# Performance work log

Measured on AMD Instinct MI355X. Metric: run time of the kernel, lower is better.

The kernel has to match this reference:

```python
import jax, jax.numpy as jnp
import numpy as np

B, N, L = 4, 64, 64
D_MODEL = 128
D_INNER = 256   # expand=2
D_STATE = 16
D_CONV = 4
DT_RANK = 8     # ceil(D_MODEL/16)
N_LAYERS = 4
EPS = 1e-5


def setup_inputs() -> dict:
    key = jax.random.key(0)
    ks = jax.random.split(key, 16)
    f = jnp.float32
    s = 0.05
    return {
        'mha_in': jax.random.normal(ks[0], (B, N, L, D_MODEL), f),
        'mamba_mask': jax.random.bernoulli(ks[1], 0.9, (B, N, L)),
        'mlp_w1': jax.random.normal(ks[2], (D_MODEL, D_MODEL), f) * s,
        'mlp_b1': jnp.zeros((D_MODEL,), f),
        'mlp_w2': jax.random.normal(ks[3], (D_MODEL, D_MODEL), f) * s,
        'mlp_b2': jnp.zeros((D_MODEL,), f),
        'in_proj_w': jax.random.normal(ks[4], (N_LAYERS, 2 * D_INNER, D_MODEL), f) * s,
        'conv_w': jax.random.normal(ks[5], (N_LAYERS, D_INNER, D_CONV), f) * s,
        'conv_b': jnp.zeros((N_LAYERS, D_INNER), f),
        'x_proj_w': jax.random.normal(ks[6], (N_LAYERS, DT_RANK + 2 * D_STATE, D_INNER), f) * s,
        'dt_proj_w': jax.random.normal(ks[7], (N_LAYERS, D_INNER, DT_RANK), f) * s,
        'dt_proj_b': jax.random.uniform(ks[8], (N_LAYERS, D_INNER), f, -4.0, -2.0),
        'A_log': jnp.log(jnp.broadcast_to(jnp.arange(1, D_STATE + 1, dtype=f), (N_LAYERS, D_INNER, D_STATE))),
        'D_skip': jnp.ones((N_LAYERS, D_INNER), f),
        'out_proj_w': jax.random.normal(ks[9], (N_LAYERS, D_MODEL, D_INNER), f) * s,
        'blk_norm_w': jnp.ones((N_LAYERS, D_MODEL), f),
        'norm_f_w': jnp.ones((D_MODEL,), f),
    }


def rmsnorm(x, w):
    # fused add-RMSNorm keeps residual in fp32; weight multiply after normalize
    x32 = x.astype(jnp.float32)
    return (x32 * jax.lax.rsqrt(jnp.mean(x32 * x32, -1, keepdims=True) + EPS)) * w


def causal_conv1d(x, w, b):
    # x: [R, L, d_inner]; depthwise causal conv (torch conv1d, padding=D_CONV-1, truncated to L)
    xp = jnp.pad(x, ((0, 0), (D_CONV - 1, 0), (0, 0)))
    y = jnp.zeros_like(x) + b
    for k in range(D_CONV):
        y = y + w[:, k] * xp[:, k:k + L, :]
    return y


def selective_scan(u, dt, A, Bm, Cm, D_sk):
    # u, dt: [R, L, d_inner]; A: [d_inner, n]; Bm, Cm: [R, L, n]
    def step(h, inputs):
        dt_t, B_t, C_t, u_t = inputs  # [R,di], [R,n], [R,n], [R,di]
        dA = jnp.exp(dt_t[..., None] * A)                       # [R,di,n]
        h = dA * h + (dt_t * u_t)[..., None] * B_t[:, None, :]  # [R,di,n]
        y = jnp.einsum('rdn,rn->rd', h, C_t)
        return h, y
    h0 = jnp.zeros((u.shape[0], A.shape[0], A.shape[1]), u.dtype)
    xs = (dt.swapaxes(0, 1), Bm.swapaxes(0, 1), Cm.swapaxes(0, 1), u.swapaxes(0, 1))
    _, ys = jax.lax.scan(step, h0, xs)
    return ys.swapaxes(0, 1) + u * D_sk


def mamba_mixer(x, in_w, conv_w, conv_b, xproj_w, dt_w, dt_b, A_log, D_sk, out_w):
    xz = x @ in_w.T                             # [R,L,2*d_inner]
    xc, z = jnp.split(xz, 2, axis=-1)
    xc = jax.nn.silu(causal_conv1d(xc, conv_w, conv_b))
    x_dbl = xc @ xproj_w.T                      # [R,L,dt_rank+2n]
    dt = jax.nn.softplus(x_dbl[..., :DT_RANK] @ dt_w.T + dt_b)
    Bm = x_dbl[..., DT_RANK:DT_RANK + D_STATE]
    Cm = x_dbl[..., DT_RANK + D_STATE:]
    A = -jnp.exp(A_log)
    y = selective_scan(xc, dt, A, Bm, Cm, D_sk)
    return (y * jax.nn.silu(z)) @ out_w.T


def _forward(mha_in, mamba_mask, mlp_w1, mlp_b1, mlp_w2, mlp_b2, in_proj_w, conv_w,
             conv_b, x_proj_w, dt_proj_w, dt_proj_b, A_log, D_skip, out_proj_w,
             blk_norm_w, norm_f_w):
    R = B * N
    x = mha_in.reshape(R, L, D_MODEL)
    key_valid = jnp.any(mamba_mask.reshape(R, L), axis=-1)
    # hist_embed_mlp: Linear -> GELU(exact) -> Linear
    h = jax.nn.gelu(x @ mlp_w1.T + mlp_b1, approximate=False) @ mlp_w2.T + mlp_b2
    residual = None
    for i in range(N_LAYERS):
        residual = h if residual is None else h + residual  # fused add (fp32 residual)
        hn = rmsnorm(residual, blk_norm_w[i])
        h = mamba_mixer(hn, in_proj_w[i], conv_w[i], conv_b[i], x_proj_w[i],
                        dt_proj_w[i], dt_proj_b[i], A_log[i], D_skip[i], out_proj_w[i])
    residual = h + residual
    out = rmsnorm(residual, norm_f_w)            # prenorm=False final fused add-norm
    # scatter into zeros over valid rows == mask-multiply (rows independent)
    out = out * key_valid[:, None, None].astype(out.dtype)
    out = out.reshape(B, N, L, D_MODEL)
    return out[:, 0, -1, :]                      # ag_feat[:, -1, :]


def reference(mha_in, mamba_mask, mlp_w1, mlp_b1, mlp_w2, mlp_b2, in_proj_w, conv_w,
              conv_b, x_proj_w, dt_proj_w, dt_proj_b, A_log, D_skip, out_proj_w,
              blk_norm_w, norm_f_w):
    return _forward(mha_in, mamba_mask, mlp_w1, mlp_b1, mlp_w2, mlp_b2, in_proj_w,
                    conv_w, conv_b, x_proj_w, dt_proj_w, dt_proj_b, A_log, D_skip,
                    out_proj_w, blk_norm_w, norm_f_w)
```

## Files before the change

### kernel.cpp

```cpp
#include <hip/hip_runtime.h>
#include <math.h>

#define NWG  64
#define NTHR 512

#define WS_XG 512
#define WS_DT (WS_XG + 65536)
#define WS_DU (WS_DT + 65536)
#define WS_BC (WS_DU + 65536)
#define WS_Y  (WS_BC + 8192)

__device__ __forceinline__ float silu_f(float v) { return v / (1.0f + __expf(-v)); }
__device__ __forceinline__ float dot4(float4 a, float4 b) {
    return a.x*b.x + a.y*b.y + a.z*b.z + a.w*b.w;
}
__device__ __forceinline__ float wave_red_sum(float v) {
    v += __shfl_xor(v, 1);  v += __shfl_xor(v, 2);  v += __shfl_xor(v, 4);
    v += __shfl_xor(v, 8);  v += __shfl_xor(v, 16); v += __shfl_xor(v, 32);
    return v;
}
__device__ __forceinline__ float aload(const float* p) {
    return __hip_atomic_load(p, __ATOMIC_RELAXED, __HIP_MEMORY_SCOPE_AGENT);
}
__device__ __forceinline__ void astore(float* p, float v) {
    __hip_atomic_store(p, v, __ATOMIC_RELAXED, __HIP_MEMORY_SCOPE_AGENT);
}

__device__ __forceinline__ void seq_barrier(unsigned* slot) {
    __syncthreads();
    if (threadIdx.x == 0) {
        asm volatile("s_waitcnt vmcnt(0)" ::: "memory");
        __hip_atomic_fetch_add(slot, 1u, __ATOMIC_RELAXED, __HIP_MEMORY_SCOPE_AGENT);
        while (__hip_atomic_load(slot, __ATOMIC_RELAXED, __HIP_MEMORY_SCOPE_AGENT) < 16u)
            __builtin_amdgcn_s_sleep(1);
    }
    __syncthreads();
}

__global__ __launch_bounds__(NTHR, 1) void fused_kernel(
    const float* __restrict__ mha_in, const int* __restrict__ mask,
    const float* __restrict__ mlp_w1, const float* __restrict__ mlp_b1,
    const float* __restrict__ mlp_w2, const float* __restrict__ mlp_b2,
    const float* __restrict__ in_proj_w, const float* __restrict__ conv_w,
    const float* __restrict__ conv_b, const float* __restrict__ x_proj_w,
    const float* __restrict__ dt_proj_w, const float* __restrict__ dt_proj_b,
    const float* __restrict__ A_log, const float* __restrict__ D_skip,
    const float* __restrict__ out_proj_w, const float* __restrict__ blk_norm_w,
    const float* __restrict__ norm_f_w,
    float* __restrict__ ws, float* __restrict__ out)
{
    const int wg = blockIdx.x;
    const int t  = threadIdx.x;
    const int s  = wg & 3;
    const int rb = wg >> 2;
    const int l0 = rb * 4;
    const int r0 = s*64 + l0;
    const int d0 = rb * 16;
    const int h  = t >> 7;
    const int c  = t & 127;
    const int wave = t >> 6;

    unsigned* bar = (unsigned*)ws;
    float* xg  = ws + WS_XG;
    float* dtg = ws + WS_DT;
    float* dug = ws + WS_DU;
    float* bcg = ws + WS_BC;
    float* yg  = ws + WS_Y;

    __shared__ float bufX[4][256];
    __shared__ float bufZ[4][256];
    __shared__ float bufA[4][256];
    __shared__ float bufG[4][256];
    __shared__ float bufB[4][128];
    __shared__ float xdS[4][40];
    __shared__ float sdt[64][17];
    __shared__ float sdu[64][17];
    __shared__ float sbc[64][33];
    __shared__ float pOut[4][4][128];
    __shared__ float part[8];
    __shared__ int   anyv;

    float resid;

    bufB[h][c] = mha_in[(size_t)s*524288 + (size_t)(l0 + h)*128 + c];
    __syncthreads();
    {
        const float* w = mlp_w1 + (size_t)c * 128;
        float acc = 0.f;
        #pragma unroll 16
        for (int k4 = 0; k4 < 32; ++k4)
            acc += dot4(*(const float4*)&bufB[h][k4*4], *(const float4*)&w[k4*4]);
        float v = acc + mlp_b1[c];
        v = 0.5f*v*(1.0f + erff(v*0.70710678118f));
        bufA[h][c] = v;
    }
    __syncthreads();
    {
        const float* w = mlp_w2 + (size_t)c * 128;
        float acc = 0.f;
        #pragma unroll 16
        for (int k4 = 0; k4 < 32; ++k4)
            acc += dot4(*(const float4*)&bufA[h][k4*4], *(const float4*)&w[k4*4]);
        resid = acc + mlp_b2[c];
    }
    __syncthreads();

    for (int layer = 0; layer < 4; ++layer) {
        unsigned* s1slot = bar + (layer*4 + s)*16;
        unsigned* s2slot = bar + 256 + layer*4 + s;
        unsigned* s3slot = bar + 272 + layer*4 + s;

        {
            float sq = wave_red_sum(resid*resid);
            if ((t & 63) == 0) part[wave] = sq;
        }
        __syncthreads();
        {
            float sr = part[h*2] + part[h*2 + 1];
            float sc = rsqrtf(sr*(1.0f/128.0f) + 1e-5f);
            bufB[h][c] = resid * sc * blk_norm_w[layer*128 + c];
        }
        __syncthreads();

        {
            const int d = t & 255, hp = t >> 8;
            const float* w = in_proj_w + ((size_t)layer*512 + d)*128;
            float a0 = 0.f, a1 = 0.f;
            #pragma unroll 16
            for (int k4 = 0; k4 < 32; ++k4) {
                float4 wv = *(const float4*)&w[k4*4];
                a0 += dot4(*(const float4*)&bufB[hp*2  ][k4*4], wv);
                a1 += dot4(*(const float4*)&bufB[hp*2+1][k4*4], wv);
            }
            bufX[hp*2  ][d] = a0;
            bufX[hp*2+1][d] = a1;
            astore(&xg[(size_t)(r0 + hp*2    )*256 + d], a0);
            astore(&xg[(size_t)(r0 + hp*2 + 1)*256 + d], a1);
        }
        __syncthreads();
        if (t == 0) {
            asm volatile("s_waitcnt vmcnt(0)" ::: "memory");
            __hip_atomic_fetch_add(s1slot + rb, 1u, __ATOMIC_RELAXED, __HIP_MEMORY_SCOPE_AGENT);
            if (rb > 0) {
                while (__hip_atomic_load(s1slot + rb - 1, __ATOMIC_RELAXED, __HIP_MEMORY_SCOPE_AGENT) == 0u)
                    __builtin_amdgcn_s_sleep(1);
            }
        }
        __syncthreads();

        {
            int d = t & 255, half = t >> 8;
            int rbase = s*64;
            float4 cw = *(const float4*)&conv_w[((size_t)layer*256 + d)*4];
            float cb = conv_b[layer*256 + d];
            if (half == 0) {
                float x0 = (l0-3 >= 0) ? aload(&xg[(size_t)(rbase+l0-3)*256 + d]) : 0.f;
                float x1 = (l0-2 >= 0) ? aload(&xg[(size_t)(rbase+l0-2)*256 + d]) : 0.f;
                float x2 = (l0-1 >= 0) ? aload(&xg[(size_t)(rbase+l0-1)*256 + d]) : 0.f;
                float x3 = bufX[0][d];
                float x4 = bufX[1][d];
                bufA[0][d] = silu_f(cb + cw.x*x0 + cw.y*x1 + cw.z*x2 + cw.w*x3);
                bufA[1][d] = silu_f(cb + cw.x*x1 + cw.y*x2 + cw.z*x3 + cw.w*x4);
            } else {
                float x0 = (l0-1 >= 0) ? aload(&xg[(size_t)(rbase+l0-1)*256 + d]) : 0.f;
                float x1 = bufX[0][d];
                float x2 = bufX[1][d];
                float x3 = bufX[2][d];
                float x4 = bufX[3][d];
                bufA[2][d] = silu_f(cb + cw.x*x0 + cw.y*x1 + cw.z*x2 + cw.w*x3);
                bufA[3][d] = silu_f(cb + cw.x*x1 + cw.y*x2 + cw.z*x3 + cw.w*x4);
            }
        }
        __syncthreads();

        if (t < 160) {
            int rq = t & 3, jx = t >> 2;
            const float* xw = x_proj_w + ((size_t)layer*40 + jx)*256;
            float acc = 0.f;
            #pragma unroll 16
            for (int k4 = 0; k4 < 64; ++k4)
                acc += dot4(*(const float4*)&bufA[rq][k4*4], *(const float4*)&xw[k4*4]);
            xdS[rq][jx] = acc;
            if (jx >= 8)
                astore(&bcg[(size_t)(r0+rq)*32 + (jx-8)], acc);
        }
        __syncthreads();

        {
            int d = t & 255, half = t >> 8;
            const float* dw = dt_proj_w + ((size_t)layer*256 + d)*8;
            float4 wa = *(const float4*)&dw[0];
            float4 wb = *(const float4*)&dw[4];
            float b = dt_proj_b[layer*256 + d];
            #pragma unroll
            for (int q = 0; q < 2; ++q) {
                int rloc = half*2 + q;
                float4 xa = *(const float4*)&xdS[rloc][0];
                float4 xb = *(const float4*)&xdS[rloc][4];
                float pre = b + dot4(xa, wa) + dot4(xb, wb);
                float sp = (pre > 20.f) ? pre : log1pf(__expf(pre));
                astore(&dtg[(size_t)(r0+rloc)*256 + d], sp);
                astore(&dug[(size_t)(r0+rloc)*256 + d], sp * bufA[rloc][d]);
            }
        }
        seq_barrier(s2slot);

        if (t < 256) {
            int l = t >> 2, q = t & 3;
            const float* p = &dtg[(size_t)(s*64+l)*256 + d0 + q*4];
            sdt[l][q*4]   = aload(p);     sdt[l][q*4+1] = aload(p+1);
            sdt[l][q*4+2] = aload(p+2);   sdt[l][q*4+3] = aload(p+3);
        } else {
            int tt = t - 256; int l = tt >> 2, q = tt & 3;
            const float* p = &dug[(size_t)(s*64+l)*256 + d0 + q*4];
            sdu[l][q*4]   = aload(p);     sdu[l][q*4+1] = aload(p+1);
            sdu[l][q*4+2] = aload(p+2);   sdu[l][q*4+3] = aload(p+3);
        }
        {
            int l = t >> 3, q = t & 7;
            const float* p = &bcg[(size_t)(s*64+l)*32 + q*4];
            sbc[l][q*4]   = aload(p);     sbc[l][q*4+1] = aload(p+1);
            sbc[l][q*4+2] = aload(p+2);   sbc[l][q*4+3] = aload(p+3);
        }
        __syncthreads();

        if (t < 64) {
            const int dloc = t >> 2, sub = t & 3, d = d0 + dloc;
            const float* Ab = A_log + ((size_t)layer*256 + d)*16 + sub*4;
            float A0 = -__expf(Ab[0]), A1 = -__expf(Ab[1]);
            float A2 = -__expf(Ab[2]), A3 = -__expf(Ab[3]);
            float h0 = 0.f, h1v = 0.f, h2v = 0.f, h3v = 0.f;
            #pragma unroll 4
            for (int l = 0; l < 64; ++l) {
                float dtv = sdt[l][dloc];
                float duv = sdu[l][dloc];
                float4 B4, C4;
                B4.x = sbc[l][sub*4];      B4.y = sbc[l][sub*4+1];
                B4.z = sbc[l][sub*4+2];    B4.w = sbc[l][sub*4+3];
                C4.x = sbc[l][16+sub*4];   C4.y = sbc[l][16+sub*4+1];
                C4.z = sbc[l][16+sub*4+2]; C4.w = sbc[l][16+sub*4+3];
                float dA, yp;
                dA = __expf(dtv*A0); h0  = dA*h0  + duv*B4.x; yp  = h0 *C4.x;
                dA = __expf(dtv*A1); h1v = dA*h1v + duv*B4.y; yp += h1v*C4.y;
                dA = __expf(dtv*A2); h2v = dA*h2v + duv*B4.z; yp += h2v*C4.z;
                dA = __expf(dtv*A3); h3v = dA*h3v + duv*B4.w; yp += h3v*C4.w;
                yp += __shfl_xor(yp, 1);
                yp += __shfl_xor(yp, 2);
                if (sub == 0) astore(&yg[(size_t)(s*64+l)*256 + d], yp);
            }
        } else if (t >= 256) {
            const int dz = t - 256;
            const float* w = in_proj_w + ((size_t)layer*512 + 256 + dz)*128;
            float a0=0.f, a1=0.f, a2=0.f, a3=0.f;
            #pragma unroll 16
            for (int k4 = 0; k4 < 32; ++k4) {
                float4 wv = *(const float4*)&w[k4*4];
                a0 += dot4(*(const float4*)&bufB[0][k4*4], wv);
                a1 += dot4(*(const float4*)&bufB[1][k4*4], wv);
                a2 += dot4(*(const float4*)&bufB[2][k4*4], wv);
                a3 += dot4(*(const float4*)&bufB[3][k4*4], wv);
            }
            bufZ[0][dz] = a0;  bufZ[1][dz] = a1;
            bufZ[2][dz] = a2;  bufZ[3][dz] = a3;
        }
        seq_barrier(s3slot);

        {
            int d = t & 255, half = t >> 8;
            float Dsk = D_skip[layer*256 + d];
            #pragma unroll
            for (int q = 0; q < 2; ++q) {
                int rloc = half*2 + q; int r = r0 + rloc;
                float z = bufZ[rloc][d];
                float yv = aload(&yg[(size_t)r*256 + d]) + bufA[rloc][d]*Dsk;
                bufG[rloc][d] = yv * silu_f(z);
            }
        }
        __syncthreads();

        {
            const int cc = t & 127, kc = t >> 7;
            const float* w = out_proj_w + ((size_t)layer*128 + cc)*256 + kc*64;
            float p0=0.f, p1=0.f, p2=0.f, p3=0.f;
            #pragma unroll
            for (int k4 = 0; k4 < 16; ++k4) {
                float4 wv = *(const float4*)&w[k4*4];
                p0 += dot4(*(const float4*)&bufG[0][kc*64 + k4*4], wv);
                p1 += dot4(*(const float4*)&bufG[1][kc*64 + k4*4], wv);
                p2 += dot4(*(const float4*)&bufG[2][kc*64 + k4*4], wv);
                p3 += dot4(*(const float4*)&bufG[3][kc*64 + k4*4], wv);
            }
            pOut[kc][0][cc] = p0;  pOut[kc][1][cc] = p1;
            pOut[kc][2][cc] = p2;  pOut[kc][3][cc] = p3;
        }
        __syncthreads();
        resid += pOut[0][h][c] + pOut[1][h][c] + pOut[2][h][c] + pOut[3][h][c];
        __syncthreads();
    }

    if (t == 0) anyv = 0;
    __syncthreads();
    if (rb == 15) {
        if (t < 64 && mask[s*4096 + t] != 0) anyv = 1;
        float sq = wave_red_sum(resid*resid);
        if ((t & 63) == 0) part[wave] = sq;
    }
    __syncthreads();
    if (rb == 15 && h == 3) {
        float sr = part[6] + part[7];
        float sc = rsqrtf(sr*(1.0f/128.0f) + 1e-5f);
        float o  = resid * sc * norm_f_w[c];
        out[s*128 + c] = anyv ? o : 0.f;
    }
}

extern "C" void kernel_launch(void* const* d_in, const int* in_sizes, int n_in,
                              void* d_out, int out_size, void* d_ws, size_t ws_size,
                              hipStream_t stream) {
    (void)in_sizes; (void)n_in; (void)out_size; (void)ws_size;
    const float* mha_in     = (const float*)d_in[0];
    const int*   mask       = (const int*)  d_in[1];
    const float* mlp_w1     = (const float*)d_in[2];
    const float* mlp_b1     = (const float*)d_in[3];
    const float* mlp_w2     = (const float*)d_in[4];
    const float* mlp_b2     = (const float*)d_in[5];
    const float* in_proj_w  = (const float*)d_in[6];
    const float* conv_w     = (const float*)d_in[7];
    const float* conv_b     = (const float*)d_in[8];
    const float* x_proj_w   = (const float*)d_in[9];
    const float* dt_proj_w  = (const float*)d_in[10];
    const float* dt_proj_b  = (const float*)d_in[11];
    const float* A_log      = (const float*)d_in[12];
    const float* D_skip     = (const float*)d_in[13];
    const float* out_proj_w = (const float*)d_in[14];
    const float* blk_norm_w = (const float*)d_in[15];
    const float* norm_f_w   = (const float*)d_in[16];
    float* ws  = (float*)d_ws;
    float* out = (float*)d_out;

    hipMemsetAsync(d_ws, 0, 2048, stream);

    fused_kernel<<<NWG, NTHR, 0, stream>>>(
        mha_in, mask, mlp_w1, mlp_b1, mlp_w2, mlp_b2,
        in_proj_w, conv_w, conv_b, x_proj_w, dt_proj_w, dt_proj_b,
        A_log, D_skip, out_proj_w, blk_norm_w, norm_f_w, ws, out);
}
```

Measured before the change: 250.3 us.

## Share normed halo rows instead of in_proj outputs and widen scan parallelism

Instead of publishing in_proj x outputs to global memory and waiting on the neighbour before the conv, each workgroup publishes its last three normalized rows. It reads the previous block's halo rows and recomputes their in_proj locally, so the global traffic is smaller and the inter-workgroup wait comes earlier and overlaps the local in_proj. The selective scan now uses 256 threads, one per (channel, state), instead of 64 threads with four states each, and does a 16-lane shuffle reduction. The costs are redundant in_proj work for the three halo rows and more shuffles per scan step.

```diff
diff --git a/kernel.cpp b/kernel.cpp
--- a/kernel.cpp
+++ b/kernel.cpp
@@ -4,8 +4,8 @@
 #define NWG  64
 #define NTHR 512
 
-#define WS_XG 512
-#define WS_DT (WS_XG + 65536)
+#define WS_HN 512
+#define WS_DT (WS_HN + 32768)
 #define WS_DU (WS_DT + 65536)
 #define WS_BC (WS_DU + 65536)
 #define WS_Y  (WS_BC + 8192)
@@ -61,13 +61,14 @@
     const int wave = t >> 6;
 
     unsigned* bar = (unsigned*)ws;
-    float* xg  = ws + WS_XG;
+    float* hng = ws + WS_HN;
     float* dtg = ws + WS_DT;
     float* dug = ws + WS_DU;
     float* bcg = ws + WS_BC;
     float* yg  = ws + WS_Y;
 
-    __shared__ float bufX[4][256];
+    __shared__ float bufX[8][256];
+    __shared__ float hnH[3][128];
     __shared__ float bufZ[4][256];
     __shared__ float bufA[4][256];
     __shared__ float bufG[4][256];
@@ -106,7 +107,7 @@
     __syncthreads();
 
     for (int layer = 0; layer < 4; ++layer) {
-        unsigned* s1slot = bar + (layer*4 + s)*16;
+        unsigned* hnslot = bar + (layer*4 + s)*16;
         unsigned* s2slot = bar + 256 + layer*4 + s;
         unsigned* s3slot = bar + 272 + layer*4 + s;
 
@@ -118,9 +119,24 @@
         {
             float sr = part[h*2] + part[h*2 + 1];
             float sc = rsqrtf(sr*(1.0f/128.0f) + 1e-5f);
-            bufB[h][c] = resid * sc * blk_norm_w[layer*128 + c];
-        }
-        __syncthreads();
+            float hv = resid * sc * blk_norm_w[layer*128 + c];
+            bufB[h][c] = hv;
+            if (h >= 1) astore(&hng[(size_t)(r0 + h)*128 + c], hv);
+        }
+        __syncthreads();
+        if (t == 0) {
+            asm volatile("s_waitcnt vmcnt(0)" ::: "memory");
+            __hip_atomic_fetch_add(hnslot + rb, 1u, __ATOMIC_RELAXED, __HIP_MEMORY_SCOPE_AGENT);
+            if (rb > 0) {
+                while (__hip_atomic_load(hnslot + rb - 1, __ATOMIC_RELAXED, __HIP_MEMORY_SCOPE_AGENT) == 0u)
+                    __builtin_amdgcn_s_sleep(1);
+            }
+        }
+        __syncthreads();
+
+        float hvH = 0.f;
+        if (rb > 0 && t < 384)
+            hvH = aload(&hng[(size_t)(r0 - 3 + (t >> 7))*128 + (t & 127)]);
 
         {
             const int d = t & 255, hp = t >> 8;
@@ -132,44 +148,42 @@
                 a0 += dot4(*(const float4*)&bufB[hp*2  ][k4*4], wv);
                 a1 += dot4(*(const float4*)&bufB[hp*2+1][k4*4], wv);
             }
-            bufX[hp*2  ][d] = a0;
-            bufX[hp*2+1][d] = a1;
-            astore(&xg[(size_t)(r0 + hp*2    )*256 + d], a0);
-            astore(&xg[(size_t)(r0 + hp*2 + 1)*256 + d], a1);
-        }
-        __syncthreads();
-        if (t == 0) {
-            asm volatile("s_waitcnt vmcnt(0)" ::: "memory");
-            __hip_atomic_fetch_add(s1slot + rb, 1u, __ATOMIC_RELAXED, __HIP_MEMORY_SCOPE_AGENT);
-            if (rb > 0) {
-                while (__hip_atomic_load(s1slot + rb - 1, __ATOMIC_RELAXED, __HIP_MEMORY_SCOPE_AGENT) == 0u)
-                    __builtin_amdgcn_s_sleep(1);
+            bufX[3 + hp*2][d] = a0;
+            bufX[4 + hp*2][d] = a1;
+        }
+        if (t < 384) hnH[t >> 7][t & 127] = hvH;
+        __syncthreads();
+
+        {
+            const int d = t & 255, hp = t >> 8;
+            const float* w = in_proj_w + ((size_t)layer*512 + d)*128;
+            float a = 0.f;
+            #pragma unroll 16
+            for (int k4 = 0; k4 < 32; ++k4)
+                a += dot4(*(const float4*)&hnH[hp][k4*4], *(const float4*)&w[k4*4]);
+            bufX[hp][d] = a;
+            if (t < 256) {
+                const float* w2 = in_proj_w + ((size_t)layer*512 + t)*128;
+                float a2 = 0.f;
+                #pragma unroll 16
+                for (int k4 = 0; k4 < 32; ++k4)
+                    a2 += dot4(*(const float4*)&hnH[2][k4*4], *(const float4*)&w2[k4*4]);
+                bufX[2][t] = a2;
             }
         }
         __syncthreads();
 
         {
             int d = t & 255, half = t >> 8;
-            int rbase = s*64;
             float4 cw = *(const float4*)&conv_w[((size_t)layer*256 + d)*4];
             float cb = conv_b[layer*256 + d];
-            if (half == 0) {
-                float x0 = (l0-3 >= 0) ? aload(&xg[(size_t)(rbase+l0-3)*256 + d]) : 0.f;
-                float x1 = (l0-2 >= 0) ? aload(&xg[(size_t)(rbase+l0-2)*256 + d]) : 0.f;
-                float x2 = (l0-1 >= 0) ? aload(&xg[(size_t)(rbase+l0-1)*256 + d]) : 0.f;
-                float x3 = bufX[0][d];
-                float x4 = bufX[1][d];
-                bufA[0][d] = silu_f(cb + cw.x*x0 + cw.y*x1 + cw.z*x2 + cw.w*x3);
-                bufA[1][d] = silu_f(cb + cw.x*x1 + cw.y*x2 + cw.z*x3 + cw.w*x4);
-            } else {
-                float x0 = (l0-1 >= 0) ? aload(&xg[(size_t)(rbase+l0-1)*256 + d]) : 0.f;
-                float x1 = bufX[0][d];
-                float x2 = bufX[1][d];
-                float x3 = bufX[2][d];
-                float x4 = bufX[3][d];
-                bufA[2][d] = silu_f(cb + cw.x*x0 + cw.y*x1 + cw.z*x2 + cw.w*x3);
-                bufA[3][d] = silu_f(cb + cw.x*x1 + cw.y*x2 + cw.z*x3 + cw.w*x4);
-            }
+            float x0 = bufX[half*2    ][d];
+            float x1 = bufX[half*2 + 1][d];
+            float x2 = bufX[half*2 + 2][d];
+            float x3 = bufX[half*2 + 3][d];
+            float x4 = bufX[half*2 + 4][d];
+            bufA[half*2    ][d] = silu_f(cb + cw.x*x0 + cw.y*x1 + cw.z*x2 + cw.w*x3);
+            bufA[half*2 + 1][d] = silu_f(cb + cw.x*x1 + cw.y*x2 + cw.z*x3 + cw.w*x4);
         }
         __syncthreads();
 
@@ -224,31 +238,29 @@
         }
         __syncthreads();
 
-        if (t < 64) {
-            const int dloc = t >> 2, sub = t & 3, d = d0 + dloc;
-            const float* Ab = A_log + ((size_t)layer*256 + d)*16 + sub*4;
-            float A0 = -__expf(Ab[0]), A1 = -__expf(Ab[1]);
-            float A2 = -__expf(Ab[2]), A3 = -__expf(Ab[3]);
-            float h0 = 0.f, h1v = 0.f, h2v = 0.f, h3v = 0.f;
+        if (t < 256) {
+            const int lane = t & 63, w4 = t >> 6;
+            const int cl = lane >> 4, n = lane & 15;
+            const int lch = w4*4 + cl;
+            const int d = d0 + lch;
+            const float A = -__expf(A_log[((size_t)(layer*256 + d))*16 + n]);
+            float hst = 0.f;
             #pragma unroll 4
             for (int l = 0; l < 64; ++l) {
-                float dtv = sdt[l][dloc];
-                float duv = sdu[l][dloc];
-                float4 B4, C4;
-                B4.x = sbc[l][sub*4];      B4.y = sbc[l][sub*4+1];
-                B4.z = sbc[l][sub*4+2];    B4.w = sbc[l][sub*4+3];
-                C4.x = sbc[l][16+sub*4];   C4.y = sbc[l][16+sub*4+1];
-                C4.z = sbc[l][16+sub*4+2]; C4.w = sbc[l][16+sub*4+3];
-                float dA, yp;
-                dA = __expf(dtv*A0); h0  = dA*h0  + duv*B4.x; yp  = h0 *C4.x;
-                dA = __expf(dtv*A1); h1v = dA*h1v + duv*B4.y; yp += h1v*C4.y;
-                dA = __expf(dtv*A2); h2v = dA*h2v + duv*B4.z; yp += h2v*C4.z;
-                dA = __expf(dtv*A3); h3v = dA*h3v + duv*B4.w; yp += h3v*C4.w;
-                yp += __shfl_xor(yp, 1);
-                yp += __shfl_xor(yp, 2);
-                if (sub == 0) astore(&yg[(size_t)(s*64+l)*256 + d], yp);
-            }
-        } else if (t >= 256) {
+                float dtv = sdt[l][lch];
+                float duv = sdu[l][lch];
+                float Bn  = sbc[l][n];
+                float Cn  = sbc[l][16 + n];
+                float dA  = __expf(dtv * A);
+                hst = dA*hst + duv*Bn;
+                float p = hst * Cn;
+                p += __shfl_xor(p, 1);
+                p += __shfl_xor(p, 2);
+                p += __shfl_xor(p, 4);
+                p += __shfl_xor(p, 8);
+                if (n == 0) astore(&yg[(size_t)(s*64+l)*256 + d], p);
+            }
+        } else {
             const int dz = t - 256;
             const float* w = in_proj_w + ((size_t)layer*512 + 256 + dz)*128;
             float a0=0.f, a1=0.f, a2=0.f, a3=0.f;
```

Result: slower. 298.8 us (+19.4%).

## Split GEMV dot products across 8-lane groups for coalesced weight loads

Applied to the files above, without the earlier changes.

Every matrix-vector product (MLP, in_proj x and z halves, x_proj, out_proj) is rewritten so an 8-lane group shares one output column. Each lane loads interleaved float4 slices of the weight row, computes all four rows, and reduces with xor shuffles. Before, each thread walked a whole weight row on its own, which gave strided, uncoalesced global loads. The new form coalesces weight reads and reuses each weight load across four rows, at the cost of extra shuffles and idle lanes during writeback. out_proj no longer needs the pOut partial-sum buffer.

```diff
diff --git a/kernel.cpp b/kernel.cpp
--- a/kernel.cpp
+++ b/kernel.cpp
@@ -18,6 +18,13 @@
     v += __shfl_xor(v, 1);  v += __shfl_xor(v, 2);  v += __shfl_xor(v, 4);
     v += __shfl_xor(v, 8);  v += __shfl_xor(v, 16); v += __shfl_xor(v, 32);
     return v;
+}
+__device__ __forceinline__ float red8(float v) {
+    v += __shfl_xor(v, 1);  v += __shfl_xor(v, 2);  v += __shfl_xor(v, 4);
+    return v;
+}
+__device__ __forceinline__ float sel4(int ln, float a0, float a1, float a2, float a3) {
+    return ln==0 ? a0 : (ln==1 ? a1 : (ln==2 ? a2 : a3));
 }
 __device__ __forceinline__ float aload(const float* p) {
     return __hip_atomic_load(p, __ATOMIC_RELAXED, __HIP_MEMORY_SCOPE_AGENT);
@@ -59,6 +66,7 @@
     const int h  = t >> 7;
     const int c  = t & 127;
     const int wave = t >> 6;
+    const int grp = t >> 3, ln = t & 7;
 
     unsigned* bar = (unsigned*)ws;
     float* xg  = ws + WS_XG;
@@ -72,11 +80,11 @@
     __shared__ float bufA[4][256];
     __shared__ float bufG[4][256];
     __shared__ float bufB[4][128];
+    __shared__ float bufR[4][128];
     __shared__ float xdS[4][40];
     __shared__ float sdt[64][17];
     __shared__ float sdu[64][17];
     __shared__ float sbc[64][33];
-    __shared__ float pOut[4][4][128];
     __shared__ float part[8];
     __shared__ int   anyv;
 
@@ -85,24 +93,52 @@
     bufB[h][c] = mha_in[(size_t)s*524288 + (size_t)(l0 + h)*128 + c];
     __syncthreads();
     {
-        const float* w = mlp_w1 + (size_t)c * 128;
-        float acc = 0.f;
-        #pragma unroll 16
-        for (int k4 = 0; k4 < 32; ++k4)
-            acc += dot4(*(const float4*)&bufB[h][k4*4], *(const float4*)&w[k4*4]);
-        float v = acc + mlp_b1[c];
-        v = 0.5f*v*(1.0f + erff(v*0.70710678118f));
-        bufA[h][c] = v;
+        #pragma unroll
+        for (int pass = 0; pass < 2; ++pass) {
+            const int j = pass*64 + grp;
+            const float* w = mlp_w1 + (size_t)j*128 + ln*4;
+            float4 wv[4];
+            #pragma unroll
+            for (int i = 0; i < 4; ++i) wv[i] = *(const float4*)&w[i*32];
+            float a0=0.f, a1=0.f, a2=0.f, a3=0.f;
+            #pragma unroll
+            for (int i = 0; i < 4; ++i) {
+                a0 += dot4(*(const float4*)&bufB[0][ln*4 + i*32], wv[i]);
+                a1 += dot4(*(const float4*)&bufB[1][ln*4 + i*32], wv[i]);
+                a2 += dot4(*(const float4*)&bufB[2][ln*4 + i*32], wv[i]);
+                a3 += dot4(*(const float4*)&bufB[3][ln*4 + i*32], wv[i]);
+            }
+            a0 = red8(a0); a1 = red8(a1); a2 = red8(a2); a3 = red8(a3);
+            if (ln < 4) {
+                float v = sel4(ln, a0, a1, a2, a3) + mlp_b1[j];
+                bufA[ln][j] = 0.5f*v*(1.0f + erff(v*0.70710678118f));
+            }
+        }
     }
     __syncthreads();
     {
-        const float* w = mlp_w2 + (size_t)c * 128;
-        float acc = 0.f;
-        #pragma unroll 16
-        for (int k4 = 0; k4 < 32; ++k4)
-            acc += dot4(*(const float4*)&bufA[h][k4*4], *(const float4*)&w[k4*4]);
-        resid = acc + mlp_b2[c];
-    }
+        #pragma unroll
+        for (int pass = 0; pass < 2; ++pass) {
+            const int j = pass*64 + grp;
+            const float* w = mlp_w2 + (size_t)j*128 + ln*4;
+            float4 wv[4];
+            #pragma unroll
+            for (int i = 0; i < 4; ++i) wv[i] = *(const float4*)&w[i*32];
+            float a0=0.f, a1=0.f, a2=0.f, a3=0.f;
+            #pragma unroll
+            for (int i = 0; i < 4; ++i) {
+                a0 += dot4(*(const float4*)&bufA[0][ln*4 + i*32], wv[i]);
+                a1 += dot4(*(const float4*)&bufA[1][ln*4 + i*32], wv[i]);
+                a2 += dot4(*(const float4*)&bufA[2][ln*4 + i*32], wv[i]);
+                a3 += dot4(*(const float4*)&bufA[3][ln*4 + i*32], wv[i]);
+            }
+            a0 = red8(a0); a1 = red8(a1); a2 = red8(a2); a3 = red8(a3);
+            if (ln < 4)
+                bufR[ln][j] = sel4(ln, a0, a1, a2, a3) + mlp_b2[j];
+        }
+    }
+    __syncthreads();
+    resid = bufR[h][c];
     __syncthreads();
 
     for (int layer = 0; layer < 4; ++layer) {
@@ -123,19 +159,28 @@
         __syncthreads();
 
         {
-            const int d = t & 255, hp = t >> 8;
-            const float* w = in_proj_w + ((size_t)layer*512 + d)*128;
-            float a0 = 0.f, a1 = 0.f;
-            #pragma unroll 16
-            for (int k4 = 0; k4 < 32; ++k4) {
-                float4 wv = *(const float4*)&w[k4*4];
-                a0 += dot4(*(const float4*)&bufB[hp*2  ][k4*4], wv);
-                a1 += dot4(*(const float4*)&bufB[hp*2+1][k4*4], wv);
-            }
-            bufX[hp*2  ][d] = a0;
-            bufX[hp*2+1][d] = a1;
-            astore(&xg[(size_t)(r0 + hp*2    )*256 + d], a0);
-            astore(&xg[(size_t)(r0 + hp*2 + 1)*256 + d], a1);
+            #pragma unroll
+            for (int pass = 0; pass < 4; ++pass) {
+                const int j = pass*64 + grp;
+                const float* w = in_proj_w + ((size_t)layer*512 + j)*128 + ln*4;
+                float4 wv[4];
+                #pragma unroll
+                for (int i = 0; i < 4; ++i) wv[i] = *(const float4*)&w[i*32];
+                float a0=0.f, a1=0.f, a2=0.f, a3=0.f;
+                #pragma unroll
+                for (int i = 0; i < 4; ++i) {
+                    a0 += dot4(*(const float4*)&bufB[0][ln*4 + i*32], wv[i]);
+                    a1 += dot4(*(const float4*)&bufB[1][ln*4 + i*32], wv[i]);
+                    a2 += dot4(*(const float4*)&bufB[2][ln*4 + i*32], wv[i]);
+                    a3 += dot4(*(const float4*)&bufB[3][ln*4 + i*32], wv[i]);
+                }
+                a0 = red8(a0); a1 = red8(a1); a2 = red8(a2); a3 = red8(a3);
+                if (ln < 4) {
+                    float v = sel4(ln, a0, a1, a2, a3);
+                    bufX[ln][j] = v;
+                    astore(&xg[(size_t)(r0 + ln)*256 + j], v);
+                }
+            }
         }
         __syncthreads();
         if (t == 0) {
@@ -173,16 +218,27 @@
         }
         __syncthreads();
 
-        if (t < 160) {
-            int rq = t & 3, jx = t >> 2;
-            const float* xw = x_proj_w + ((size_t)layer*40 + jx)*256;
-            float acc = 0.f;
-            #pragma unroll 16
-            for (int k4 = 0; k4 < 64; ++k4)
-                acc += dot4(*(const float4*)&bufA[rq][k4*4], *(const float4*)&xw[k4*4]);
-            xdS[rq][jx] = acc;
-            if (jx >= 8)
-                astore(&bcg[(size_t)(r0+rq)*32 + (jx-8)], acc);
+        if (t < 320) {
+            const int jx = grp;
+            const float* xw = x_proj_w + ((size_t)layer*40 + jx)*256 + ln*4;
+            float4 wv[8];
+            #pragma unroll
+            for (int i = 0; i < 8; ++i) wv[i] = *(const float4*)&xw[i*32];
+            float a0=0.f, a1=0.f, a2=0.f, a3=0.f;
+            #pragma unroll
+            for (int i = 0; i < 8; ++i) {
+                a0 += dot4(*(const float4*)&bufA[0][ln*4 + i*32], wv[i]);
+                a1 += dot4(*(const float4*)&bufA[1][ln*4 + i*32], wv[i]);
+                a2 += dot4(*(const float4*)&bufA[2][ln*4 + i*32], wv[i]);
+                a3 += dot4(*(const float4*)&bufA[3][ln*4 + i*32], wv[i]);
+            }
+            a0 = red8(a0); a1 = red8(a1); a2 = red8(a2); a3 = red8(a3);
+            if (ln < 4) {
+                float v = sel4(ln, a0, a1, a2, a3);
+                xdS[ln][jx] = v;
+                if (jx >= 8)
+                    astore(&bcg[(size_t)(r0+ln)*32 + (jx-8)], v);
+            }
         }
         __syncthreads();
 
@@ -249,19 +305,29 @@
                 if (sub == 0) astore(&yg[(size_t)(s*64+l)*256 + d], yp);
             }
         } else if (t >= 256) {
-            const int dz = t - 256;
-            const float* w = in_proj_w + ((size_t)layer*512 + 256 + dz)*128;
-            float a0=0.f, a1=0.f, a2=0.f, a3=0.f;
-            #pragma unroll 16
-            for (int k4 = 0; k4 < 32; ++k4) {
-                float4 wv = *(const float4*)&w[k4*4];
-                a0 += dot4(*(const float4*)&bufB[0][k4*4], wv);
-                a1 += dot4(*(const float4*)&bufB[1][k4*4], wv);
-                a2 += dot4(*(const float4*)&bufB[2][k4*4], wv);
-                a3 += dot4(*(const float4*)&bufB[3][k4*4], wv);
-            }
-            bufZ[0][dz] = a0;  bufZ[1][dz] = a1;
-            bufZ[2][dz] = a2;  bufZ[3][dz] = a3;
+            const int tz = t - 256, gz = tz >> 3, lz = tz & 7;
+            #pragma unroll 2
+            for (int pass = 0; pass < 8; ++pass) {
+                const int j = pass*32 + gz;
+                const float* w = in_proj_w + ((size_t)layer*512 + 256 + j)*128 + lz*4;
+                float4 wv[4];
+                #pragma unroll
+                for (int i = 0; i < 4; ++i) wv[i] = *(const float4*)&w[i*32];
+                float a0=0.f, a1=0.f, a2=0.f, a3=0.f;
+                #pragma unroll
+                for (int i = 0; i < 4; ++i) {
+                    a0 += dot4(*(const float4*)&bufB[0][lz*4 + i*32], wv[i]);
+                    a1 += dot4(*(const float4*)&bufB[1][lz*4 + i*32], wv[i]);
+                    a2 += dot4(*(const float4*)&bufB[2][lz*4 + i*32], wv[i]);
+                    a3 += dot4(*(const float4*)&bufB[3][lz*4 + i*32], wv[i]);
+                }
+                a0 += __shfl_xor(a0, 1); a0 += __shfl_xor(a0, 2); a0 += __shfl_xor(a0, 4);
+                a1 += __shfl_xor(a1, 1); a1 += __shfl_xor(a1, 2); a1 += __shfl_xor(a1, 4);
+                a2 += __shfl_xor(a2, 1); a2 += __shfl_xor(a2, 2); a2 += __shfl_xor(a2, 4);
+                a3 += __shfl_xor(a3, 1); a3 += __shfl_xor(a3, 2); a3 += __shfl_xor(a3, 4);
+                if (lz < 4)
+                    bufZ[lz][j] = sel4(lz, a0, a1, a2, a3);
+            }
         }
         seq_barrier(s3slot);
 
@@ -279,22 +345,28 @@
         __syncthreads();
 
         {
-            const int cc = t & 127, kc = t >> 7;
-            const float* w = out_proj_w + ((size_t)layer*128 + cc)*256 + kc*64;
-            float p0=0.f, p1=0.f, p2=0.f, p3=0.f;
-            #pragma unroll
-            for (int k4 = 0; k4 < 16; ++k4) {
-                float4 wv = *(const float4*)&w[k4*4];
-                p0 += dot4(*(const float4*)&bufG[0][kc*64 + k4*4], wv);
-                p1 += dot4(*(const float4*)&bufG[1][kc*64 + k4*4], wv);
-                p2 += dot4(*(const float4*)&bufG[2][kc*64 + k4*4], wv);
-                p3 += dot4(*(const float4*)&bufG[3][kc*64 + k4*4], wv);
-            }
-            pOut[kc][0][cc] = p0;  pOut[kc][1][cc] = p1;
-            pOut[kc][2][cc] = p2;  pOut[kc][3][cc] = p3;
-        }
-        __syncthreads();
-        resid += pOut[0][h][c] + pOut[1][h][c] + pOut[2][h][c] + pOut[3][h][c];
+            #pragma unroll
+            for (int pass = 0; pass < 2; ++pass) {
+                const int j = pass*64 + grp;
+                const float* w = out_proj_w + ((size_t)layer*128 + j)*256 + ln*4;
+                float4 wv[8];
+                #pragma unroll
+                for (int i = 0; i < 8; ++i) wv[i] = *(const float4*)&w[i*32];
+                float a0=0.f, a1=0.f, a2=0.f, a3=0.f;
+                #pragma unroll
+                for (int i = 0; i < 8; ++i) {
+                    a0 += dot4(*(const float4*)&bufG[0][ln*4 + i*32], wv[i]);
+                    a1 += dot4(*(const float4*)&bufG[1][ln*4 + i*32], wv[i]);
+                    a2 += dot4(*(const float4*)&bufG[2][ln*4 + i*32], wv[i]);
+                    a3 += dot4(*(const float4*)&bufG[3][ln*4 + i*32], wv[i]);
+                }
+                a0 = red8(a0); a1 = red8(a1); a2 = red8(a2); a3 = red8(a3);
+                if (ln < 4)
+                    bufR[ln][j] = sel4(ln, a0, a1, a2, a3);
+            }
+        }
+        __syncthreads();
+        resid += bufR[h][c];
         __syncthreads();
     }
 
```

After: 210.0 us. 16.1% less time.
